# Performance work log

Measured on AMD Instinct MI355X. Metric: run time of the kernel, lower is better.

Reference implementation:

```python
import jax, jax.numpy as jnp
import numpy as np


def _quant(x):
    # Per-tensor dynamic uint8 quantization to produce LUT row/col indices.
    # (The CUDA kernel's exact requant scheme is not in the source; this is the
    # assumed scheme: scale so max |x| -> 255, round, clip to [0,255].)
    s = 255.0 / jnp.maximum(jnp.max(jnp.abs(x)), jnp.float32(1e-6))
    return jnp.clip(jnp.round(x * s), 0, 255).astype(jnp.int32)


def _lut_conv(x, w, b, lut):
    # CustomAnyConv2d: stride=1, padding=(2,2), kernel 5x5.
    O, Cin, kh, kw = w.shape
    # im2col patches: (B, Cin*kh*kw, H, W), feature ordering matches w.reshape(O, -1)
    patches = jax.lax.conv_general_dilated_patches(
        x, (kh, kw), (1, 1), ((2, 2), (2, 2)))
    B, K, H, W = patches.shape
    pi = _quant(patches).reshape(B, K, H * W)            # (B,K,P)
    wi = _quant(w.reshape(O, K))                          # (O,K)
    vals = lut[pi[:, None, :, :], wi[None, :, :, None]]   # (B,O,K,P) gather
    out = vals.sum(axis=2).reshape(B, O, H, W)            # accumulate LUT products
    return out + b[None, :, None, None]


def _lut_dense(x, w, b, lut):
    # CustomAnyDense: out[h, o] = sum_k LUT[x[h,k], w[o,k]] + b[o]
    xi = _quant(x)                                        # (B,K)
    wi = _quant(w)                                        # (O,K)
    vals = lut[xi[:, None, :], wi[None, :, :]]            # (B,O,K)
    return vals.sum(axis=2) + b


def _maxpool2(x, pad=0):
    return jax.lax.reduce_window(
        x, -jnp.inf, jax.lax.max,
        (1, 1, 2, 2), (1, 1, 2, 2),
        ((0, 0), (0, 0), (pad, pad), (pad, pad)))


def setup_inputs() -> dict:
    key = jax.random.key(0)
    ks = jax.random.split(key, 11)
    B = 32
    x = jax.random.uniform(ks[0], (B, 1, 28, 28), jnp.float32)
    ij = np.arange(256)
    # Approximate-multiplier LUT: high byte of exact 8x8-bit product (uint8-valued).
    lut = jnp.asarray(((ij[:, None] * ij[None, :]) >> 8).astype(np.float32))
    return {
        "x": x,
        "lut": lut,
        "w1": jax.random.uniform(ks[1], (16, 1, 5, 5), jnp.float32),
        "b1": jax.random.normal(ks[2], (16,), jnp.float32) * 0.01,
        "w2": jax.random.uniform(ks[3], (32, 16, 5, 5), jnp.float32),
        "b2": jax.random.normal(ks[4], (32,), jnp.float32) * 0.01,
        "w3": jax.random.uniform(ks[5], (64, 32, 5, 5), jnp.float32),
        "b3": jax.random.normal(ks[6], (64,), jnp.float32) * 0.01,
        "fw1": jax.random.uniform(ks[7], (256, 1024), jnp.float32),
        "fb1": jax.random.normal(ks[8], (256,), jnp.float32) * 0.01,
        "fw2": jax.random.uniform(ks[9], (10, 256), jnp.float32),
        "fb2": jax.random.normal(ks[10], (10,), jnp.float32) * 0.01,
    }


def reference(x, lut, w1, b1, w2, b2, w3, b3, fw1, fb1, fw2, fb2):
    h = jax.nn.relu(_lut_conv(x, w1, b1, lut))
    h = _maxpool2(h)                     # (B,16,14,14)
    h = jax.nn.relu(_lut_conv(h, w2, b2, lut))
    h = _maxpool2(h)                     # (B,32,7,7)
    h = jax.nn.relu(_lut_conv(h, w3, b3, lut))
    h = _maxpool2(h, pad=1)              # (B,64,4,4)
    h = h.reshape(h.shape[0], -1)        # (B,1024)
    h = jax.nn.relu(_lut_dense(h, fw1, fb1, lut))
    h = _lut_dense(h, fw2, fb2, lut)     # (B,10)
    return jax.nn.log_softmax(h, axis=1)
```

## Files before the change

kernel.cpp:

```cpp
#include <hip/hip_runtime.h>
#include <math.h>

typedef unsigned int  u32;
typedef unsigned short u16;
typedef unsigned short u16x2 __attribute__((ext_vector_type(2)));

#define O_A1     4096
#define O_A2     405504
#define O_A3     606208
#define O_A4     737280

__device__ __forceinline__ float blk_max(float v, float* red) {
  int t = threadIdx.x;
  __syncthreads();
  red[t] = v;
  __syncthreads();
#pragma unroll
  for (int s = 128; s > 0; s >>= 1) {
    if (t < s) red[t] = fmaxf(red[t], red[t + s]);
    __syncthreads();
  }
  return red[0];
}

__device__ __forceinline__ void amax_f(float* slot, float v) {
  atomicMax((int*)slot, (int)__float_as_uint(v));
}

__device__ __forceinline__ u16 quant1(float v, float s) {
  float q = rintf(v * s);
  q = fminf(fmaxf(q, 0.0f), 255.0f);
  return (u16)q;
}

__device__ __forceinline__ void mac_u32(u32& acc, u32 a, u32 w) {
  u16x2 av = __builtin_bit_cast(u16x2, a);
  u16x2 wv = __builtin_bit_cast(u16x2, w);
  u16x2 p  = av * wv;
  acc += (__builtin_bit_cast(u32, p) >> 8) & 0x00FF00FFu;
}
__device__ __forceinline__ void mac4(u32& acc, uint4 a, uint4 w) {
  mac_u32(acc, a.x, w.x); mac_u32(acc, a.y, w.y);
  mac_u32(acc, a.z, w.z); mac_u32(acc, a.w, w.w);
}

__device__ __forceinline__ float fmax4(float4 v) {
  return fmaxf(fmaxf(fabsf(v.x), fabsf(v.y)), fmaxf(fabsf(v.z), fabsf(v.w)));
}

__global__ __launch_bounds__(256) void k_conv1(
    const float* __restrict__ x, const float* __restrict__ w1, const float* __restrict__ b1,
    const float* __restrict__ w2, const float* __restrict__ w3,
    const float* __restrict__ fw1, const float* __restrict__ fw2,
    float* __restrict__ a1, float* wsf) {
  __shared__ unsigned char sx[1024];
  __shared__ u16 sw[64];
  __shared__ float red[256];
  const int t = threadIdx.x, bid = blockIdx.x;

  if (bid >= 256) {
    int sb = bid - 256;
    const float* p; int n4, base, nb, slot;
    if (sb < 2)       { p = w2;  n4 = 3200;  base = sb;      nb = 2;  slot = 2; }
    else if (sb < 10) { p = w3;  n4 = 12800; base = sb - 2;  nb = 8;  slot = 3; }
    else if (sb < 58) { p = fw1; n4 = 65536; base = sb - 10; nb = 48; slot = 4; }
    else              { p = fw2; n4 = 640;   base = 0;       nb = 1;  slot = 5; }
    const float4* p4 = (const float4*)p;
    float m = 0.f;
    for (int i = base * 256 + t; i < n4; i += nb * 256) m = fmaxf(m, fmax4(p4[i]));
    m = blk_max(m, red);
    if (t == 0) amax_f(wsf + slot, m);
    return;
  }

  int b = bid >> 3, op = bid & 7;
  float m = 0.f;
  const float4* x4 = (const float4*)x;
  for (int i = t; i < 6272; i += 256) m = fmaxf(m, fmax4(x4[i]));
  float xmax = blk_max(m, red);
  m = 0.f;
  if (t < 100) m = fmax4(((const float4*)w1)[t]);
  float w1max = blk_max(m, red);
  float s0  = 255.0f / fmaxf(xmax, 1e-6f);
  float sw1 = 255.0f / fmaxf(w1max, 1e-6f);

  u32* sxz = (u32*)sx;
  for (int i = t; i < 256; i += 256) sxz[i] = 0;
  __syncthreads();
  for (int i = t; i < 784; i += 256) {
    int y = i / 28, xx = i - y * 28;
    sx[(y + 2) * 32 + xx + 2] = (unsigned char)quant1(x[b * 784 + i], s0);
  }
  if (t < 50) sw[t] = quant1(w1[op * 50 + t], sw1);
  __syncthreads();
  float lm = 0.f;
  if (t < 196) {
    int py = t / 14, px = t - py * 14;
#pragma unroll
    for (int ol = 0; ol < 2; ++ol) {
      int oc = op * 2 + ol;
      int best = -2147483647;
#pragma unroll
      for (int dy = 0; dy < 2; ++dy)
#pragma unroll
        for (int dx = 0; dx < 2; ++dx) {
          int cy = 2 * py + dy, cx = 2 * px + dx;
          int acc = 0;
#pragma unroll
          for (int kh = 0; kh < 5; ++kh) {
            const unsigned char* xp = sx + (cy + kh) * 32 + cx;
#pragma unroll
            for (int kw = 0; kw < 5; ++kw)
              acc += ((int)xp[kw] * (int)sw[ol * 25 + kh * 5 + kw]) >> 8;
          }
          best = max(best, acc);
        }
      float v = fmaxf(0.f, (float)best + b1[oc]);
      a1[b * 3136 + t * 16 + oc] = v;
      lm = fmaxf(lm, v);
    }
  }
  lm = blk_max(lm, red);
  if (t == 0) amax_f(wsf + 6, lm);
}

__global__ __launch_bounds__(256) void k_conv2(
    const float* __restrict__ a1, const float* __restrict__ w2, const float* __restrict__ b2,
    float* __restrict__ a2, float* wsf) {
  __shared__ __align__(16) u16 sa[324 * 16];
  __shared__ __align__(16) u16 sw[800];
  __shared__ int sconv[196];
  __shared__ float red[256];
  const int t = threadIdx.x, bid = blockIdx.x;
  int b = bid >> 4, og = bid & 15;
  float s1 = 255.0f / fmaxf(wsf[6], 1e-6f);
  float sw2 = 255.0f / fmaxf(wsf[2], 1e-6f);
  u32* sz = (u32*)sa;
  for (int i = t; i < 2592; i += 256) sz[i] = 0;
  __syncthreads();
  for (int i = t; i < 3136; i += 256) {
    int px = i >> 4, c = i & 15;
    int y = px / 14, xx = px - y * 14;
    sa[((y + 2) * 18 + xx + 2) * 16 + c] = quant1(a1[b * 3136 + i], s1);
  }
  for (int i = t; i < 800; i += 256) {
    int ol = i / 400, r = i - ol * 400, c = r / 25, tp = r - c * 25;
    sw[ol * 400 + tp * 16 + c] = quant1(w2[(og * 2 + ol) * 400 + c * 25 + tp], sw2);
  }
  __syncthreads();
  int h = t & 1, pxb = t >> 1;
  float lm = 0.f;
  for (int ol = 0; ol < 2; ++ol) {
    int oc = og * 2 + ol;
    const uint4* wq = (const uint4*)(sw + ol * 400);
#pragma unroll
    for (int rep = 0; rep < 2; ++rep) {
      int px = pxb + rep * 128;
      if (px < 196) {
        int y = px / 14, xx = px - y * 14;
        u32 acc = 0;
#pragma unroll
        for (int kh = 0; kh < 5; ++kh)
#pragma unroll
          for (int kw = 0; kw < 5; ++kw) {
            int row = (y + kh) * 18 + (xx + kw);
            uint4 av = *(const uint4*)(sa + row * 16 + h * 8);
            mac4(acc, av, wq[(kh * 5 + kw) * 2 + h]);
          }
        int ai = (int)((acc & 0xFFFFu) + (acc >> 16));
        ai += __shfl_down(ai, 1, 2);
        if (h == 0) sconv[px] = ai;
      }
    }
    __syncthreads();
    if (t < 49) {
      int py = t / 7, px = t - py * 7;
      int mm = sconv[(2 * py) * 14 + 2 * px];
      mm = max(mm, sconv[(2 * py) * 14 + 2 * px + 1]);
      mm = max(mm, sconv[(2 * py + 1) * 14 + 2 * px]);
      mm = max(mm, sconv[(2 * py + 1) * 14 + 2 * px + 1]);
      float v = fmaxf(0.f, (float)mm + b2[oc]);
      a2[b * 1568 + t * 32 + oc] = v;
      lm = fmaxf(lm, v);
    }
    __syncthreads();
  }
  lm = blk_max(lm, red);
  if (t == 0) amax_f(wsf + 7, lm);
}

__global__ __launch_bounds__(256) void k_conv3(
    const float* __restrict__ a2, const float* __restrict__ w3, const float* __restrict__ b3,
    float* __restrict__ a3, float* wsf) {
  __shared__ __align__(16) u16 sa[121 * 40];
  __shared__ __align__(16) u16 sw[4 * 800];
  __shared__ float red[256];
  const int t = threadIdx.x, bid = blockIdx.x;
  int b = bid >> 4, og = bid & 15;
  float s2 = 255.0f / fmaxf(wsf[7], 1e-6f);
  float sw3 = 255.0f / fmaxf(wsf[3], 1e-6f);
  u32* sz = (u32*)sa;
  for (int i = t; i < 2420; i += 256) sz[i] = 0;
  __syncthreads();
  for (int i = t; i < 1568; i += 256) {
    int px = i >> 5, c = i & 31;
    int y = px / 7, xx = px - y * 7;
    sa[((y + 2) * 11 + xx + 2) * 40 + c] = quant1(a2[b * 1568 + i], s2);
  }
  for (int i = t; i < 3200; i += 256) {
    int ol = i / 800, r = i - ol * 800, c = r / 25, tp = r - c * 25;
    sw[ol * 800 + tp * 32 + c] = quant1(w3[(og * 4 + ol) * 800 + c * 25 + tp], sw3);
  }
  __syncthreads();
  int q = t & 3, pos = t >> 2;
  int dydx = pos & 3, r = pos >> 2;
  int py = r >> 2, px = r & 3;
  int cy = 2 * py - 1 + (dydx >> 1), cx = 2 * px - 1 + (dydx & 1);
  bool valid = (cy >= 0 && cy < 7 && cx >= 0 && cx < 7);
  float lm = 0.f;
  for (int ol = 0; ol < 4; ++ol) {
    int oc = og * 4 + ol;
    int ai = 0;
    if (valid) {
      u32 acc = 0;
#pragma unroll
      for (int kh = 0; kh < 5; ++kh)
#pragma unroll
        for (int kw = 0; kw < 5; ++kw) {
          int row = (cy + kh) * 11 + (cx + kw);
          uint4 av = *(const uint4*)(sa + row * 40 + q * 8);
          uint4 wv = *(const uint4*)(sw + ol * 800 + (kh * 5 + kw) * 32 + q * 8);
          mac4(acc, av, wv);
        }
      ai = (int)((acc & 0xFFFFu) + (acc >> 16));
    }
    ai += __shfl_down(ai, 2, 4);
    ai += __shfl_down(ai, 1, 4);
    int val = valid ? ai : -(1 << 30);
    int mm = max(val, __shfl_down(val, 4, 16));
    mm = max(mm, __shfl_down(mm, 8, 16));
    if ((t & 15) == 0) {
      float v = fmaxf(0.f, (float)mm + b3[oc]);
      a3[b * 1024 + oc * 16 + r] = v;
      lm = fmaxf(lm, v);
    }
  }
  lm = blk_max(lm, red);
  if (t == 0) amax_f(wsf + 8, lm);
}

__global__ __launch_bounds__(256) void k_dense1(
    const float* __restrict__ a3f, const float* __restrict__ fw1, const float* __restrict__ fb1,
    float* __restrict__ a4, float* wsf) {
  __shared__ __align__(16) u16 sh[1024];
  __shared__ float red[256];
  const int t = threadIdx.x, bid = blockIdx.x;
  int b = bid >> 4, og = bid & 15;
  float s3 = 255.0f / fmaxf(wsf[8], 1e-6f);
  float sws = 255.0f / fmaxf(wsf[4], 1e-6f);
  for (int i = t; i < 1024; i += 256)
    sh[i] = quant1(a3f[b * 1024 + i], s3);
  __syncthreads();
  int ol = t >> 4, ks = t & 15;
  int o = og * 16 + ol;
  const float4* wf = (const float4*)(fw1 + o * 1024);
  const uint4* hp = (const uint4*)sh;
  u32 acc = 0;
#pragma unroll
  for (int j = 0; j < 8; ++j) {
    int e = j * 16 + ks;
    float4 f0 = wf[e * 2], f1 = wf[e * 2 + 1];
    uint4 wv;
    wv.x = (u32)quant1(f0.x, sws) | ((u32)quant1(f0.y, sws) << 16);
    wv.y = (u32)quant1(f0.z, sws) | ((u32)quant1(f0.w, sws) << 16);
    wv.z = (u32)quant1(f1.x, sws) | ((u32)quant1(f1.y, sws) << 16);
    wv.w = (u32)quant1(f1.z, sws) | ((u32)quant1(f1.w, sws) << 16);
    mac4(acc, hp[e], wv);
  }
  int ai = (int)((acc & 0xFFFFu) + (acc >> 16));
#pragma unroll
  for (int d = 8; d > 0; d >>= 1)
    ai += __shfl_down(ai, d, 16);
  float lm = 0.f;
  if (ks == 0) {
    float v = fmaxf(0.f, (float)ai + fb1[o]);
    a4[b * 256 + o] = v;
    lm = v;
  }
  lm = blk_max(lm, red);
  if (t == 0) amax_f(wsf + 9, lm);
}

__global__ __launch_bounds__(64) void k_dense2(
    const float* __restrict__ a4, const float* __restrict__ fw2, const float* __restrict__ fb2,
    float* __restrict__ out, float* wsf) {
  int b = blockIdx.x;
  __shared__ __align__(16) u16 sh[256];
  __shared__ float z[16];
  int t = threadIdx.x;
  float s4 = 255.0f / fmaxf(wsf[9], 1e-6f);
  float sws = 255.0f / fmaxf(wsf[5], 1e-6f);
  for (int i = t; i < 256; i += 64)
    sh[i] = quant1(a4[b * 256 + i], s4);
  __syncthreads();
  if (t < 40) {
    int o = t >> 2, ks = t & 3;
    const float4* wf = (const float4*)(fw2 + o * 256);
    const uint4* hp = (const uint4*)sh;
    u32 acc = 0;
#pragma unroll
    for (int j = 0; j < 8; ++j) {
      int e = j * 4 + ks;
      float4 f0 = wf[e * 2], f1 = wf[e * 2 + 1];
      uint4 wv;
      wv.x = (u32)quant1(f0.x, sws) | ((u32)quant1(f0.y, sws) << 16);
      wv.y = (u32)quant1(f0.z, sws) | ((u32)quant1(f0.w, sws) << 16);
      wv.z = (u32)quant1(f1.x, sws) | ((u32)quant1(f1.y, sws) << 16);
      wv.w = (u32)quant1(f1.z, sws) | ((u32)quant1(f1.w, sws) << 16);
      mac4(acc, hp[e], wv);
    }
    int ai = (int)((acc & 0xFFFFu) + (acc >> 16));
    ai += __shfl_down(ai, 2, 4);
    ai += __shfl_down(ai, 1, 4);
    if (ks == 0) z[o] = (float)ai + fb2[o];
  }
  __syncthreads();
  if (t < 10) {
    float m = z[0];
#pragma unroll
    for (int j = 1; j < 10; ++j) m = fmaxf(m, z[j]);
    float se = 0.f;
#pragma unroll
    for (int j = 0; j < 10; ++j) se += expf(z[j] - m);
    out[b * 10 + t] = z[t] - (m + logf(se));
  }
}

extern "C" void kernel_launch(void* const* d_in, const int* in_sizes, int n_in,
                              void* d_out, int out_size, void* d_ws, size_t ws_size,
                              hipStream_t stream) {
  const float* x   = (const float*)d_in[0];
  const float* w1  = (const float*)d_in[2];
  const float* b1  = (const float*)d_in[3];
  const float* w2  = (const float*)d_in[4];
  const float* b2  = (const float*)d_in[5];
  const float* w3  = (const float*)d_in[6];
  const float* b3  = (const float*)d_in[7];
  const float* fw1 = (const float*)d_in[8];
  const float* fb1 = (const float*)d_in[9];
  const float* fw2 = (const float*)d_in[10];
  const float* fb2 = (const float*)d_in[11];
  float* out = (float*)d_out;
  unsigned char* ws8 = (unsigned char*)d_ws;
  float* wsf = (float*)d_ws;
  float* A1 = (float*)(ws8 + O_A1);
  float* A2 = (float*)(ws8 + O_A2);
  float* A3 = (float*)(ws8 + O_A3);
  float* A4 = (float*)(ws8 + O_A4);

  k_conv1 <<<315, 256, 0, stream>>>(x, w1, b1, w2, w3, fw1, fw2, A1, wsf);
  k_conv2 <<<512, 256, 0, stream>>>(A1, w2, b2, A2, wsf);
  k_conv3 <<<512, 256, 0, stream>>>(A2, w3, b3, A3, wsf);
  k_dense1<<<512, 256, 0, stream>>>(A3, fw1, fb1, A4, wsf);
  k_dense2<<<32, 64, 0, stream>>>(A4, fw2, fb2, out, wsf);
}
```

Baseline: 139.7 us.

## Fuse all five layer kernels into one cooperative kernel with grid syncs

Replaces the five separate kernel launches with one cooperative kernel of 512 blocks that runs each layer in turn, separated by grid.sync(), with shared memory overlaid through a union. The aim is to remove per-launch overhead and inter-kernel gaps. In exchange, every stage now has to fit the same 512x256 grid, all blocks must be co-resident for the cooperative launch, and each grid-wide barrier has its own cost. Amax reductions across stages still depend on atomics completing before each grid.sync.

New measurement: 344.2 us. 146% more time.

```diff
diff --git a/kernel.cpp b/kernel.cpp
--- a/kernel.cpp
+++ b/kernel.cpp
@@ -1,5 +1,8 @@
 #include <hip/hip_runtime.h>
+#include <hip/hip_cooperative_groups.h>
 #include <math.h>
+
+namespace cg = cooperative_groups;
 
 typedef unsigned int  u32;
 typedef unsigned short u16;
@@ -48,269 +51,223 @@
   return fmaxf(fmaxf(fabsf(v.x), fabsf(v.y)), fmaxf(fabsf(v.z), fabsf(v.w)));
 }
 
-__global__ __launch_bounds__(256) void k_conv1(
-    const float* __restrict__ x, const float* __restrict__ w1, const float* __restrict__ b1,
-    const float* __restrict__ w2, const float* __restrict__ w3,
-    const float* __restrict__ fw1, const float* __restrict__ fw2,
-    float* __restrict__ a1, float* wsf) {
-  __shared__ unsigned char sx[1024];
-  __shared__ u16 sw[64];
+__global__ __launch_bounds__(256, 2) void k_fused(
+    const float* __restrict__ x,
+    const float* __restrict__ w1, const float* __restrict__ b1,
+    const float* __restrict__ w2, const float* __restrict__ b2,
+    const float* __restrict__ w3, const float* __restrict__ b3,
+    const float* __restrict__ fw1, const float* __restrict__ fb1,
+    const float* __restrict__ fw2, const float* __restrict__ fb2,
+    float* __restrict__ a1, float* __restrict__ a2,
+    float* __restrict__ a3, float* __restrict__ a4,
+    float* __restrict__ out, float* wsf) {
+  __shared__ __align__(16) union {
+    struct { unsigned char sx[1024]; u16 sw[64]; } c1;
+    struct { u16 sa[324 * 16]; u16 sw[800]; int sconv[196]; } c2;
+    struct { u16 sa[121 * 40]; u16 sw[3200]; } c3;
+    struct { u16 sh[1024]; } d1;
+    struct { u16 sh[256]; float z[16]; } d2;
+  } sm;
   __shared__ float red[256];
   const int t = threadIdx.x, bid = blockIdx.x;
+  cg::grid_group grid = cg::this_grid();
 
   if (bid >= 256) {
-    int sb = bid - 256;
-    const float* p; int n4, base, nb, slot;
-    if (sb < 2)       { p = w2;  n4 = 3200;  base = sb;      nb = 2;  slot = 2; }
-    else if (sb < 10) { p = w3;  n4 = 12800; base = sb - 2;  nb = 8;  slot = 3; }
-    else if (sb < 58) { p = fw1; n4 = 65536; base = sb - 10; nb = 48; slot = 4; }
-    else              { p = fw2; n4 = 640;   base = 0;       nb = 1;  slot = 5; }
-    const float4* p4 = (const float4*)p;
+    if (bid < 315) {
+      int sb = bid - 256;
+      const float* p; int n4, base, nb, slot;
+      if (sb < 2)       { p = w2;  n4 = 3200;  base = sb;      nb = 2;  slot = 2; }
+      else if (sb < 10) { p = w3;  n4 = 12800; base = sb - 2;  nb = 8;  slot = 3; }
+      else if (sb < 58) { p = fw1; n4 = 65536; base = sb - 10; nb = 48; slot = 4; }
+      else              { p = fw2; n4 = 640;   base = 0;       nb = 1;  slot = 5; }
+      const float4* p4 = (const float4*)p;
+      float m = 0.f;
+      for (int i = base * 256 + t; i < n4; i += nb * 256) m = fmaxf(m, fmax4(p4[i]));
+      m = blk_max(m, red);
+      if (t == 0) amax_f(wsf + slot, m);
+    }
+  } else {
+    int b = bid >> 3, op = bid & 7;
     float m = 0.f;
-    for (int i = base * 256 + t; i < n4; i += nb * 256) m = fmaxf(m, fmax4(p4[i]));
-    m = blk_max(m, red);
-    if (t == 0) amax_f(wsf + slot, m);
-    return;
-  }
-
-  int b = bid >> 3, op = bid & 7;
-  float m = 0.f;
-  const float4* x4 = (const float4*)x;
-  for (int i = t; i < 6272; i += 256) m = fmaxf(m, fmax4(x4[i]));
-  float xmax = blk_max(m, red);
-  m = 0.f;
-  if (t < 100) m = fmax4(((const float4*)w1)[t]);
-  float w1max = blk_max(m, red);
-  float s0  = 255.0f / fmaxf(xmax, 1e-6f);
-  float sw1 = 255.0f / fmaxf(w1max, 1e-6f);
-
-  u32* sxz = (u32*)sx;
-  for (int i = t; i < 256; i += 256) sxz[i] = 0;
-  __syncthreads();
-  for (int i = t; i < 784; i += 256) {
-    int y = i / 28, xx = i - y * 28;
-    sx[(y + 2) * 32 + xx + 2] = (unsigned char)quant1(x[b * 784 + i], s0);
-  }
-  if (t < 50) sw[t] = quant1(w1[op * 50 + t], sw1);
-  __syncthreads();
-  float lm = 0.f;
-  if (t < 196) {
-    int py = t / 14, px = t - py * 14;
-#pragma unroll
+    const float4* x4 = (const float4*)x;
+    for (int i = t; i < 6272; i += 256) m = fmaxf(m, fmax4(x4[i]));
+    float xmax = blk_max(m, red);
+    m = 0.f;
+    if (t < 100) m = fmax4(((const float4*)w1)[t]);
+    float w1max = blk_max(m, red);
+    float s0  = 255.0f / fmaxf(xmax, 1e-6f);
+    float sw1 = 255.0f / fmaxf(w1max, 1e-6f);
+
+    u32* sxz = (u32*)sm.c1.sx;
+    for (int i = t; i < 256; i += 256) sxz[i] = 0;
+    __syncthreads();
+    for (int i = t; i < 784; i += 256) {
+      int y = i / 28, xx = i - y * 28;
+      sm.c1.sx[(y + 2) * 32 + xx + 2] = (unsigned char)quant1(x[b * 784 + i], s0);
+    }
+    if (t < 50) sm.c1.sw[t] = quant1(w1[op * 50 + t], sw1);
+    __syncthreads();
+    float lm = 0.f;
+    if (t < 196) {
+      int py = t / 14, px = t - py * 14;
+#pragma unroll
+      for (int ol = 0; ol < 2; ++ol) {
+        int oc = op * 2 + ol;
+        int best = -2147483647;
+#pragma unroll
+        for (int dy = 0; dy < 2; ++dy)
+#pragma unroll
+          for (int dx = 0; dx < 2; ++dx) {
+            int cy = 2 * py + dy, cx = 2 * px + dx;
+            int acc = 0;
+#pragma unroll
+            for (int kh = 0; kh < 5; ++kh) {
+              const unsigned char* xp = sm.c1.sx + (cy + kh) * 32 + cx;
+#pragma unroll
+              for (int kw = 0; kw < 5; ++kw)
+                acc += ((int)xp[kw] * (int)sm.c1.sw[ol * 25 + kh * 5 + kw]) >> 8;
+            }
+            best = max(best, acc);
+          }
+        float v = fmaxf(0.f, (float)best + b1[oc]);
+        a1[b * 3136 + t * 16 + oc] = v;
+        lm = fmaxf(lm, v);
+      }
+    }
+    lm = blk_max(lm, red);
+    if (t == 0) amax_f(wsf + 6, lm);
+  }
+  grid.sync();
+
+  {
+    int b = bid >> 4, og = bid & 15;
+    float s1 = 255.0f / fmaxf(wsf[6], 1e-6f);
+    float sw2s = 255.0f / fmaxf(wsf[2], 1e-6f);
+    u32* sz = (u32*)sm.c2.sa;
+    for (int i = t; i < 2592; i += 256) sz[i] = 0;
+    __syncthreads();
+    for (int i = t; i < 3136; i += 256) {
+      int px = i >> 4, c = i & 15;
+      int y = px / 14, xx = px - y * 14;
+      sm.c2.sa[((y + 2) * 18 + xx + 2) * 16 + c] = quant1(a1[b * 3136 + i], s1);
+    }
+    for (int i = t; i < 800; i += 256) {
+      int ol = i / 400, r = i - ol * 400, c = r / 25, tp = r - c * 25;
+      sm.c2.sw[ol * 400 + tp * 16 + c] = quant1(w2[(og * 2 + ol) * 400 + c * 25 + tp], sw2s);
+    }
+    __syncthreads();
+    int h = t & 1, pxb = t >> 1;
+    float lm = 0.f;
     for (int ol = 0; ol < 2; ++ol) {
-      int oc = op * 2 + ol;
-      int best = -2147483647;
-#pragma unroll
-      for (int dy = 0; dy < 2; ++dy)
-#pragma unroll
-        for (int dx = 0; dx < 2; ++dx) {
-          int cy = 2 * py + dy, cx = 2 * px + dx;
-          int acc = 0;
-#pragma unroll
-          for (int kh = 0; kh < 5; ++kh) {
-            const unsigned char* xp = sx + (cy + kh) * 32 + cx;
-#pragma unroll
-            for (int kw = 0; kw < 5; ++kw)
-              acc += ((int)xp[kw] * (int)sw[ol * 25 + kh * 5 + kw]) >> 8;
+      int oc = og * 2 + ol;
+      const uint4* wq = (const uint4*)(sm.c2.sw + ol * 400);
+#pragma unroll
+      for (int rep = 0; rep < 2; ++rep) {
+        int px = pxb + rep * 128;
+        if (px < 196) {
+          int y = px / 14, xx = px - y * 14;
+          u32 acc = 0;
+#pragma unroll
+          for (int kh = 0; kh < 5; ++kh)
+#pragma unroll
+            for (int kw = 0; kw < 5; ++kw) {
+              int row = (y + kh) * 18 + (xx + kw);
+              uint4 av = *(const uint4*)(sm.c2.sa + row * 16 + h * 8);
+              mac4(acc, av, wq[(kh * 5 + kw) * 2 + h]);
+            }
+          int ai = (int)((acc & 0xFFFFu) + (acc >> 16));
+          ai += __shfl_down(ai, 1, 2);
+          if (h == 0) sm.c2.sconv[px] = ai;
+        }
+      }
+      __syncthreads();
+      if (t < 49) {
+        int py = t / 7, px = t - py * 7;
+        int mm = sm.c2.sconv[(2 * py) * 14 + 2 * px];
+        mm = max(mm, sm.c2.sconv[(2 * py) * 14 + 2 * px + 1]);
+        mm = max(mm, sm.c2.sconv[(2 * py + 1) * 14 + 2 * px]);
+        mm = max(mm, sm.c2.sconv[(2 * py + 1) * 14 + 2 * px + 1]);
+        float v = fmaxf(0.f, (float)mm + b2[oc]);
+        a2[b * 1568 + t * 32 + oc] = v;
+        lm = fmaxf(lm, v);
+      }
+      __syncthreads();
+    }
+    lm = blk_max(lm, red);
+    if (t == 0) amax_f(wsf + 7, lm);
+  }
+  grid.sync();
+
+  {
+    int b = bid >> 4, og = bid & 15;
+    float s2 = 255.0f / fmaxf(wsf[7], 1e-6f);
+    float sw3s = 255.0f / fmaxf(wsf[3], 1e-6f);
+    u32* sz = (u32*)sm.c3.sa;
+    for (int i = t; i < 2420; i += 256) sz[i] = 0;
+    __syncthreads();
+    for (int i = t; i < 1568; i += 256) {
+      int px = i >> 5, c = i & 31;
+      int y = px / 7, xx = px - y * 7;
+      sm.c3.sa[((y + 2) * 11 + xx + 2) * 40 + c] = quant1(a2[b * 1568 + i], s2);
+    }
+    for (int i = t; i < 3200; i += 256) {
+      int ol = i / 800, r = i - ol * 800, c = r / 25, tp = r - c * 25;
+      sm.c3.sw[ol * 800 + tp * 32 + c] = quant1(w3[(og * 4 + ol) * 800 + c * 25 + tp], sw3s);
+    }
+    __syncthreads();
+    int q = t & 3, pos = t >> 2;
+    int dydx = pos & 3, r = pos >> 2;
+    int py = r >> 2, px = r & 3;
+    int cy = 2 * py - 1 + (dydx >> 1), cx = 2 * px - 1 + (dydx & 1);
+    bool valid = (cy >= 0 && cy < 7 && cx >= 0 && cx < 7);
+    float lm = 0.f;
+    for (int ol = 0; ol < 4; ++ol) {
+      int oc = og * 4 + ol;
+      int ai = 0;
+      if (valid) {
+        u32 acc = 0;
+#pragma unroll
+        for (int kh = 0; kh < 5; ++kh)
+#pragma unroll
+          for (int kw = 0; kw < 5; ++kw) {
+            int row = (cy + kh) * 11 + (cx + kw);
+            uint4 av = *(const uint4*)(sm.c3.sa + row * 40 + q * 8);
+            uint4 wv = *(const uint4*)(sm.c3.sw + ol * 800 + (kh * 5 + kw) * 32 + q * 8);
+            mac4(acc, av, wv);
           }
-          best = max(best, acc);
-        }
-      float v = fmaxf(0.f, (float)best + b1[oc]);
-      a1[b * 3136 + t * 16 + oc] = v;
-      lm = fmaxf(lm, v);
-    }
-  }
-  lm = blk_max(lm, red);
-  if (t == 0) amax_f(wsf + 6, lm);
-}
-
-__global__ __launch_bounds__(256) void k_conv2(
-    const float* __restrict__ a1, const float* __restrict__ w2, const float* __restrict__ b2,
-    float* __restrict__ a2, float* wsf) {
-  __shared__ __align__(16) u16 sa[324 * 16];
-  __shared__ __align__(16) u16 sw[800];
-  __shared__ int sconv[196];
-  __shared__ float red[256];
-  const int t = threadIdx.x, bid = blockIdx.x;
-  int b = bid >> 4, og = bid & 15;
-  float s1 = 255.0f / fmaxf(wsf[6], 1e-6f);
-  float sw2 = 255.0f / fmaxf(wsf[2], 1e-6f);
-  u32* sz = (u32*)sa;
-  for (int i = t; i < 2592; i += 256) sz[i] = 0;
-  __syncthreads();
-  for (int i = t; i < 3136; i += 256) {
-    int px = i >> 4, c = i & 15;
-    int y = px / 14, xx = px - y * 14;
-    sa[((y + 2) * 18 + xx + 2) * 16 + c] = quant1(a1[b * 3136 + i], s1);
-  }
-  for (int i = t; i < 800; i += 256) {
-    int ol = i / 400, r = i - ol * 400, c = r / 25, tp = r - c * 25;
-    sw[ol * 400 + tp * 16 + c] = quant1(w2[(og * 2 + ol) * 400 + c * 25 + tp], sw2);
-  }
-  __syncthreads();
-  int h = t & 1, pxb = t >> 1;
-  float lm = 0.f;
-  for (int ol = 0; ol < 2; ++ol) {
-    int oc = og * 2 + ol;
-    const uint4* wq = (const uint4*)(sw + ol * 400);
-#pragma unroll
-    for (int rep = 0; rep < 2; ++rep) {
-      int px = pxb + rep * 128;
-      if (px < 196) {
-        int y = px / 14, xx = px - y * 14;
-        u32 acc = 0;
-#pragma unroll
-        for (int kh = 0; kh < 5; ++kh)
-#pragma unroll
-          for (int kw = 0; kw < 5; ++kw) {
-            int row = (y + kh) * 18 + (xx + kw);
-            uint4 av = *(const uint4*)(sa + row * 16 + h * 8);
-            mac4(acc, av, wq[(kh * 5 + kw) * 2 + h]);
-          }
-        int ai = (int)((acc & 0xFFFFu) + (acc >> 16));
-        ai += __shfl_down(ai, 1, 2);
-        if (h == 0) sconv[px] = ai;
-      }
-    }
-    __syncthreads();
-    if (t < 49) {
-      int py = t / 7, px = t - py * 7;
-      int mm = sconv[(2 * py) * 14 + 2 * px];
-      mm = max(mm, sconv[(2 * py) * 14 + 2 * px + 1]);
-      mm = max(mm, sconv[(2 * py + 1) * 14 + 2 * px]);
-      mm = max(mm, sconv[(2 * py + 1) * 14 + 2 * px + 1]);
-      float v = fmaxf(0.f, (float)mm + b2[oc]);
-      a2[b * 1568 + t * 32 + oc] = v;
-      lm = fmaxf(lm, v);
-    }
-    __syncthreads();
-  }
-  lm = blk_max(lm, red);
-  if (t == 0) amax_f(wsf + 7, lm);
-}
-
-__global__ __launch_bounds__(256) void k_conv3(
-    const float* __restrict__ a2, const float* __restrict__ w3, const float* __restrict__ b3,
-    float* __restrict__ a3, float* wsf) {
-  __shared__ __align__(16) u16 sa[121 * 40];
-  __shared__ __align__(16) u16 sw[4 * 800];
-  __shared__ float red[256];
-  const int t = threadIdx.x, bid = blockIdx.x;
-  int b = bid >> 4, og = bid & 15;
-  float s2 = 255.0f / fmaxf(wsf[7], 1e-6f);
-  float sw3 = 255.0f / fmaxf(wsf[3], 1e-6f);
-  u32* sz = (u32*)sa;
-  for (int i = t; i < 2420; i += 256) sz[i] = 0;
-  __syncthreads();
-  for (int i = t; i < 1568; i += 256) {
-    int px = i >> 5, c = i & 31;
-    int y = px / 7, xx = px - y * 7;
-    sa[((y + 2) * 11 + xx + 2) * 40 + c] = quant1(a2[b * 1568 + i], s2);
-  }
-  for (int i = t; i < 3200; i += 256) {
-    int ol = i / 800, r = i - ol * 800, c = r / 25, tp = r - c * 25;
-    sw[ol * 800 + tp * 32 + c] = quant1(w3[(og * 4 + ol) * 800 + c * 25 + tp], sw3);
-  }
-  __syncthreads();
-  int q = t & 3, pos = t >> 2;
-  int dydx = pos & 3, r = pos >> 2;
-  int py = r >> 2, px = r & 3;
-  int cy = 2 * py - 1 + (dydx >> 1), cx = 2 * px - 1 + (dydx & 1);
-  bool valid = (cy >= 0 && cy < 7 && cx >= 0 && cx < 7);
-  float lm = 0.f;
-  for (int ol = 0; ol < 4; ++ol) {
-    int oc = og * 4 + ol;
-    int ai = 0;
-    if (valid) {
-      u32 acc = 0;
-#pragma unroll
-      for (int kh = 0; kh < 5; ++kh)
-#pragma unroll
-        for (int kw = 0; kw < 5; ++kw) {
-          int row = (cy + kh) * 11 + (cx + kw);
-          uint4 av = *(const uint4*)(sa + row * 40 + q * 8);
-          uint4 wv = *(const uint4*)(sw + ol * 800 + (kh * 5 + kw) * 32 + q * 8);
-          mac4(acc, av, wv);
-        }
-      ai = (int)((acc & 0xFFFFu) + (acc >> 16));
-    }
-    ai += __shfl_down(ai, 2, 4);
-    ai += __shfl_down(ai, 1, 4);
-    int val = valid ? ai : -(1 << 30);
-    int mm = max(val, __shfl_down(val, 4, 16));
-    mm = max(mm, __shfl_down(mm, 8, 16));
-    if ((t & 15) == 0) {
-      float v = fmaxf(0.f, (float)mm + b3[oc]);
-      a3[b * 1024 + oc * 16 + r] = v;
-      lm = fmaxf(lm, v);
-    }
-  }
-  lm = blk_max(lm, red);
-  if (t == 0) amax_f(wsf + 8, lm);
-}
-
-__global__ __launch_bounds__(256) void k_dense1(
-    const float* __restrict__ a3f, const float* __restrict__ fw1, const float* __restrict__ fb1,
-    float* __restrict__ a4, float* wsf) {
-  __shared__ __align__(16) u16 sh[1024];
-  __shared__ float red[256];
-  const int t = threadIdx.x, bid = blockIdx.x;
-  int b = bid >> 4, og = bid & 15;
-  float s3 = 255.0f / fmaxf(wsf[8], 1e-6f);
-  float sws = 255.0f / fmaxf(wsf[4], 1e-6f);
-  for (int i = t; i < 1024; i += 256)
-    sh[i] = quant1(a3f[b * 1024 + i], s3);
-  __syncthreads();
-  int ol = t >> 4, ks = t & 15;
-  int o = og * 16 + ol;
-  const float4* wf = (const float4*)(fw1 + o * 1024);
-  const uint4* hp = (const uint4*)sh;
-  u32 acc = 0;
-#pragma unroll
-  for (int j = 0; j < 8; ++j) {
-    int e = j * 16 + ks;
-    float4 f0 = wf[e * 2], f1 = wf[e * 2 + 1];
-    uint4 wv;
-    wv.x = (u32)quant1(f0.x, sws) | ((u32)quant1(f0.y, sws) << 16);
-    wv.y = (u32)quant1(f0.z, sws) | ((u32)quant1(f0.w, sws) << 16);
-    wv.z = (u32)quant1(f1.x, sws) | ((u32)quant1(f1.y, sws) << 16);
-    wv.w = (u32)quant1(f1.z, sws) | ((u32)quant1(f1.w, sws) << 16);
-    mac4(acc, hp[e], wv);
-  }
-  int ai = (int)((acc & 0xFFFFu) + (acc >> 16));
-#pragma unroll
-  for (int d = 8; d > 0; d >>= 1)
-    ai += __shfl_down(ai, d, 16);
-  float lm = 0.f;
-  if (ks == 0) {
-    float v = fmaxf(0.f, (float)ai + fb1[o]);
-    a4[b * 256 + o] = v;
-    lm = v;
-  }
-  lm = blk_max(lm, red);
-  if (t == 0) amax_f(wsf + 9, lm);
-}
-
-__global__ __launch_bounds__(64) void k_dense2(
-    const float* __restrict__ a4, const float* __restrict__ fw2, const float* __restrict__ fb2,
-    float* __restrict__ out, float* wsf) {
-  int b = blockIdx.x;
-  __shared__ __align__(16) u16 sh[256];
-  __shared__ float z[16];
-  int t = threadIdx.x;
-  float s4 = 255.0f / fmaxf(wsf[9], 1e-6f);
-  float sws = 255.0f / fmaxf(wsf[5], 1e-6f);
-  for (int i = t; i < 256; i += 64)
-    sh[i] = quant1(a4[b * 256 + i], s4);
-  __syncthreads();
-  if (t < 40) {
-    int o = t >> 2, ks = t & 3;
-    const float4* wf = (const float4*)(fw2 + o * 256);
-    const uint4* hp = (const uint4*)sh;
+        ai = (int)((acc & 0xFFFFu) + (acc >> 16));
+      }
+      ai += __shfl_down(ai, 2, 4);
+      ai += __shfl_down(ai, 1, 4);
+      int val = valid ? ai : -(1 << 30);
+      int mm = max(val, __shfl_down(val, 4, 16));
+      mm = max(mm, __shfl_down(mm, 8, 16));
+      if ((t & 15) == 0) {
+        float v = fmaxf(0.f, (float)mm + b3[oc]);
+        a3[b * 1024 + oc * 16 + r] = v;
+        lm = fmaxf(lm, v);
+      }
+    }
+    lm = blk_max(lm, red);
+    if (t == 0) amax_f(wsf + 8, lm);
+  }
+  grid.sync();
+
+  {
+    int b = bid >> 4, og = bid & 15;
+    float s3 = 255.0f / fmaxf(wsf[8], 1e-6f);
+    float sws = 255.0f / fmaxf(wsf[4], 1e-6f);
+    for (int i = t; i < 1024; i += 256)
+      sm.d1.sh[i] = quant1(a3[b * 1024 + i], s3);
+    __syncthreads();
+    int ol = t >> 4, ks = t & 15;
+    int o = og * 16 + ol;
+    const float4* wf = (const float4*)(fw1 + o * 1024);
+    const uint4* hp = (const uint4*)sm.d1.sh;
     u32 acc = 0;
 #pragma unroll
     for (int j = 0; j < 8; ++j) {
-      int e = j * 4 + ks;
+      int e = j * 16 + ks;
       float4 f0 = wf[e * 2], f1 = wf[e * 2 + 1];
       uint4 wv;
       wv.x = (u32)quant1(f0.x, sws) | ((u32)quant1(f0.y, sws) << 16);
@@ -320,19 +277,57 @@
       mac4(acc, hp[e], wv);
     }
     int ai = (int)((acc & 0xFFFFu) + (acc >> 16));
-    ai += __shfl_down(ai, 2, 4);
-    ai += __shfl_down(ai, 1, 4);
-    if (ks == 0) z[o] = (float)ai + fb2[o];
-  }
-  __syncthreads();
-  if (t < 10) {
-    float m = z[0];
-#pragma unroll
-    for (int j = 1; j < 10; ++j) m = fmaxf(m, z[j]);
-    float se = 0.f;
-#pragma unroll
-    for (int j = 0; j < 10; ++j) se += expf(z[j] - m);
-    out[b * 10 + t] = z[t] - (m + logf(se));
+#pragma unroll
+    for (int d = 8; d > 0; d >>= 1)
+      ai += __shfl_down(ai, d, 16);
+    float lm = 0.f;
+    if (ks == 0) {
+      float v = fmaxf(0.f, (float)ai + fb1[o]);
+      a4[b * 256 + o] = v;
+      lm = v;
+    }
+    lm = blk_max(lm, red);
+    if (t == 0) amax_f(wsf + 9, lm);
+  }
+  grid.sync();
+
+  if (bid < 32) {
+    int b = bid;
+    float s4 = 255.0f / fmaxf(wsf[9], 1e-6f);
+    float sws = 255.0f / fmaxf(wsf[5], 1e-6f);
+    sm.d2.sh[t] = quant1(a4[b * 256 + t], s4);
+    __syncthreads();
+    if (t < 40) {
+      int o = t >> 2, ks = t & 3;
+      const float4* wf = (const float4*)(fw2 + o * 256);
+      const uint4* hp = (const uint4*)sm.d2.sh;
+      u32 acc = 0;
+#pragma unroll
+      for (int j = 0; j < 8; ++j) {
+        int e = j * 4 + ks;
+        float4 f0 = wf[e * 2], f1 = wf[e * 2 + 1];
+        uint4 wv;
+        wv.x = (u32)quant1(f0.x, sws) | ((u32)quant1(f0.y, sws) << 16);
+        wv.y = (u32)quant1(f0.z, sws) | ((u32)quant1(f0.w, sws) << 16);
+        wv.z = (u32)quant1(f1.x, sws) | ((u32)quant1(f1.y, sws) << 16);
+        wv.w = (u32)quant1(f1.z, sws) | ((u32)quant1(f1.w, sws) << 16);
+        mac4(acc, hp[e], wv);
+      }
+      int ai = (int)((acc & 0xFFFFu) + (acc >> 16));
+      ai += __shfl_down(ai, 2, 4);
+      ai += __shfl_down(ai, 1, 4);
+      if (ks == 0) sm.d2.z[o] = (float)ai + fb2[o];
+    }
+    __syncthreads();
+    if (t < 10) {
+      float mz = sm.d2.z[0];
+#pragma unroll
+      for (int j = 1; j < 10; ++j) mz = fmaxf(mz, sm.d2.z[j]);
+      float se = 0.f;
+#pragma unroll
+      for (int j = 0; j < 10; ++j) se += expf(sm.d2.z[j] - mz);
+      out[b * 10 + t] = sm.d2.z[t] - (mz + logf(se));
+    }
   }
 }
 
@@ -353,14 +348,16 @@
   float* out = (float*)d_out;
   unsigned char* ws8 = (unsigned char*)d_ws;
   float* wsf = (float*)d_ws;
-  float* A1 = (float*)(ws8 + O_A1);
-  float* A2 = (float*)(ws8 + O_A2);
-  float* A3 = (float*)(ws8 + O_A3);
-  float* A4 = (float*)(ws8 + O_A4);
-
-  k_conv1 <<<315, 256, 0, stream>>>(x, w1, b1, w2, w3, fw1, fw2, A1, wsf);
-  k_conv2 <<<512, 256, 0, stream>>>(A1, w2, b2, A2, wsf);
-  k_conv3 <<<512, 256, 0, stream>>>(A2, w3, b3, A3, wsf);
-  k_dense1<<<512, 256, 0, stream>>>(A3, fw1, fb1, A4, wsf);
-  k_dense2<<<32, 64, 0, stream>>>(A4, fw2, fb2, out, wsf);
-}
+  const float* A1c = (const float*)(ws8 + O_A1);
+  const float* A2c = (const float*)(ws8 + O_A2);
+  const float* A3c = (const float*)(ws8 + O_A3);
+  const float* A4c = (const float*)(ws8 + O_A4);
+  float* A1 = (float*)A1c; float* A2 = (float*)A2c;
+  float* A3 = (float*)A3c; float* A4 = (float*)A4c;
+
+  void* args[] = { &x, &w1, &b1, &w2, &b2, &w3, &b3,
+                   &fw1, &fb1, &fw2, &fb2,
+                   &A1, &A2, &A3, &A4, &out, &wsf };
+  hipLaunchCooperativeKernel((const void*)k_fused, dim3(512), dim3(256),
+                             args, 0, stream);
+}
```
